# Optimization experiments

Hardware: AMD Instinct MI355X
Metric: run time of the kernel (lower is better)

## Reference

```python
import jax, jax.numpy as jnp
import numpy as np

N = 50000   # nodes
E = 800000  # edges
D = 128     # input_dim == hidden_dim
R = 8       # num_relations
B = 2       # num_blocks


def setup_inputs() -> dict:
    key = jax.random.key(0)
    ks = jax.random.split(key, 9)
    x = jax.random.normal(ks[0], (N, D), dtype=jnp.float32)
    edge_index = jax.random.randint(ks[1], (2, E), 0, N, dtype=jnp.int32)
    edge_type = jax.random.randint(ks[2], (E,), 0, R, dtype=jnp.int32)
    s_blk = 1.0 / np.sqrt(D // B)
    s_root = 1.0 / np.sqrt(D)
    W1 = jax.random.normal(ks[3], (R, B, D // B, D // B), dtype=jnp.float32) * s_blk
    root1 = jax.random.normal(ks[4], (D, D), dtype=jnp.float32) * s_root
    b1 = jnp.zeros((D,), dtype=jnp.float32)
    W2 = jax.random.normal(ks[5], (R, B, D // B, D // B), dtype=jnp.float32) * s_blk
    root2 = jax.random.normal(ks[6], (D, D), dtype=jnp.float32) * s_root
    b2 = jnp.zeros((D,), dtype=jnp.float32)
    return {"x": x, "edge_index": edge_index, "edge_type": edge_type,
            "W1": W1, "root1": root1, "b1": b1,
            "W2": W2, "root2": root2, "b2": b2}


def rgcn_conv(x, src, dst, etype, W, root, bias):
    # PyG RGCNConv (num_blocks mode): per-relation MEAN aggregation of source
    # features, block-diagonal transform, summed over relations, plus root + bias.
    # Transform is linear, so aggregate first (saves per-edge matmuls).
    n = x.shape[0]
    r, b, ib, ob = W.shape
    xs = x[src]                                   # [E, d_in] gather
    seg = dst * r + etype                          # fused (node, relation) id
    sums = jax.ops.segment_sum(xs, seg, num_segments=n * r)        # [n*r, d_in]
    cnt = jax.ops.segment_sum(jnp.ones((xs.shape[0],), xs.dtype), seg,
                              num_segments=n * r)                   # [n*r]
    mean = sums / jnp.maximum(cnt, 1.0)[:, None]   # zero where no edges
    agg = mean.reshape(n, r, b, ib)                # [n, R, blocks, in/blocks]
    out = jnp.einsum('nrbc,rbcd->nbd', agg, W).reshape(n, b * ob)
    return out + x @ root + bias


def reference(x, edge_index, edge_type, W1, root1, b1, W2, root2, b2):
    src, dst = edge_index[0], edge_index[1]
    h = jax.nn.relu(rgcn_conv(x, src, dst, edge_type, W1, root1, b1))
    # dropout(p=0.2) is identity in eval mode (reference uses eval semantics)
    return rgcn_conv(h, src, dst, edge_type, W2, root2, b2)
```

## Files before the change

kernel.cpp:

```cpp
#include <hip/hip_runtime.h>

#define NN 50000
#define EE 800000
#define DD 128
#define RR 8
#define CELLS (NN * RR)
#define TILE_N 64
#define NBLK ((NN + TILE_N - 1) / TILE_N)
#define SCAN_CHUNK 1024
#define SCAN_BLOCKS ((CELLS + SCAN_CHUNK - 1) / SCAN_CHUNK)

typedef __attribute__((ext_vector_type(4))) float f32x4;
typedef __attribute__((ext_vector_type(8))) short s16x8;
union ABu { uint4 q; s16x8 v; };


__device__ __forceinline__ unsigned int packbf2(float a, float b) {
    unsigned int ua = __float_as_uint(a);
    unsigned int ub = __float_as_uint(b);
    ua = (ua + 0x7fffu + ((ua >> 16) & 1u)) >> 16;
    ub = (ub + 0x7fffu + ((ub >> 16) & 1u)) & 0xffff0000u;
    return ua | ub;
}

__device__ __forceinline__ void upadd16(float* sA, uint4 a, uint4 b) {
    unsigned int u[8] = {a.x, a.y, a.z, a.w, b.x, b.y, b.z, b.w};
#pragma unroll
    for (int j = 0; j < 8; ++j) {
        sA[2 * j]     += __uint_as_float(u[j] << 16);
        sA[2 * j + 1] += __uint_as_float(u[j] & 0xffff0000u);
    }
}

#define NB_A ((NN * 32 + 255) / 256)
#define NB_B 128
#define NB_C 32
#define NB_D ((EE + 255) / 256)

__global__ void prep_fused(const float* __restrict__ x, unsigned int* __restrict__ xb,
                           const float* __restrict__ W1, const float* __restrict__ W2,
                           unsigned int* __restrict__ Wb1, unsigned int* __restrict__ Wb2,
                           const float* __restrict__ r1, const float* __restrict__ r2,
                           unsigned int* __restrict__ rb1, unsigned int* __restrict__ rb2,
                           const int* __restrict__ dst, const int* __restrict__ et,
                           int* __restrict__ cnt) {
    int bid = blockIdx.x, tid = threadIdx.x;
    if (bid < NB_A) {
        int i = bid * 256 + tid;
        if (i < NN * 32) {
            float4 v = ((const float4*)x)[i];
            ((uint2*)xb)[i] = make_uint2(packbf2(v.x, v.y), packbf2(v.z, v.w));
        }
    } else if (bid < NB_A + NB_B) {
        int i = (bid - NB_A) * 256 + tid;
        int kp = i & 31, n = (i >> 5) & 63, rb = i >> 11;
        int s0 = (rb * 64 + 2 * kp) * 64 + n;
        int s1 = (rb * 64 + 2 * kp + 1) * 64 + n;
        Wb1[((rb * 64 + n) * 32) + kp] = packbf2(W1[s0], W1[s1]);
        Wb2[((rb * 64 + n) * 32) + kp] = packbf2(W2[s0], W2[s1]);
    } else if (bid < NB_A + NB_B + NB_C) {
        int i = (bid - NB_A - NB_B) * 256 + tid;
        int kp = i & 63, n = i >> 6;
        int s0 = (2 * kp) * 128 + n, s1 = (2 * kp + 1) * 128 + n;
        rb1[n * 64 + kp] = packbf2(r1[s0], r1[s1]);
        rb2[n * 64 + kp] = packbf2(r2[s0], r2[s1]);
    } else {
        int e = (bid - NB_A - NB_B - NB_C) * 256 + tid;
        if (e < EE) atomicAdd(&cnt[et[e] * NN + dst[e]], 1);
    }
}


__global__ __launch_bounds__(256) void scan1(const int* __restrict__ cnt,
                                             int* __restrict__ off, int* __restrict__ bsum) {
    __shared__ int s[256];
    int tid = threadIdx.x;
    int base = blockIdx.x * SCAN_CHUNK + tid * 4;
    int v[4];
#pragma unroll
    for (int i = 0; i < 4; ++i) v[i] = (base + i < CELLS) ? cnt[base + i] : 0;
    int tot = v[0] + v[1] + v[2] + v[3];
    s[tid] = tot;
    __syncthreads();
    for (int d = 1; d < 256; d <<= 1) {
        int t = (tid >= d) ? s[tid - d] : 0;
        __syncthreads();
        s[tid] += t;
        __syncthreads();
    }
    int excl = s[tid] - tot;
    if (tid == 255) bsum[blockIdx.x] = s[255];
    int run = excl;
#pragma unroll
    for (int i = 0; i < 4; ++i) {
        if (base + i < CELLS) off[base + i] = run;
        run += v[i];
    }
}

__global__ __launch_bounds__(256) void scan3(int* __restrict__ off, const int* __restrict__ bsum,
                                             int* __restrict__ cur) {
    __shared__ int red[256];
    int tid = threadIdx.x, bid = blockIdx.x;
    int a = 0;
    for (int i = tid; i < bid; i += 256) a += bsum[i];
    red[tid] = a;
    __syncthreads();
#pragma unroll
    for (int d = 128; d > 0; d >>= 1) {
        if (tid < d) red[tid] += red[tid + d];
        __syncthreads();
    }
    int add = red[0];
    int base = bid * SCAN_CHUNK + tid * 4;
#pragma unroll
    for (int i = 0; i < 4; ++i) {
        int c = base + i;
        if (c < CELLS) {
            int o = off[c] + add;
            off[c] = o;
            cur[c] = o;
        }
    }
    if (bid == 0 && tid == 0) off[CELLS] = EE;
}

__global__ void cell_scatter(const int* __restrict__ src, const int* __restrict__ dst,
                             const int* __restrict__ et, int* __restrict__ cur,
                             int* __restrict__ esrc) {
    int e = blockIdx.x * blockDim.x + threadIdx.x;
    if (e < EE) {
        int cell = et[e] * NN + dst[e];
        int pos = atomicAdd(&cur[cell], 1);
        esrc[pos] = src[e];
    }
}

template <int RELU, int WRITEF, int WRITEB>
__global__ __launch_bounds__(512, 4) void layer_fused(
    const unsigned int* __restrict__ xgb, const int* __restrict__ esrc,
    const int* __restrict__ off,
    const unsigned int* __restrict__ Wb, const unsigned int* __restrict__ rootb,
    const float* __restrict__ bias, float* __restrict__ outf,
    unsigned int* __restrict__ outb) {

    __shared__ unsigned int SH[8320];
    unsigned int* MT = SH;

    int tid = threadIdx.x;
    int n0 = blockIdx.x * TILE_N;
    int e = tid & 63, q = tid >> 6;
    int w = tid >> 6, l = tid & 63;
    int quad = l >> 4, li = l & 15;
    int b = w >> 2;

    f32x4 acc[4];
    {
        float bb = bias[16 * w + li];
#pragma unroll
        for (int mt = 0; mt < 4; ++mt) {
            acc[mt][0] = bb; acc[mt][1] = bb; acc[mt][2] = bb; acc[mt][3] = bb;
        }
    }

    int node = n0 + e;

    for (int r = 0; r < RR; ++r) {
        float sA[16];
#pragma unroll
        for (int i = 0; i < 16; ++i) sA[i] = 0.f;
        int ne = 0;
        if (node < NN) {
            int cell = r * NN + node;
            int o = off[cell];
            ne = off[cell + 1] - o;
            int t2 = 0;
            for (; t2 + 2 <= ne; t2 += 2) {
                int s0 = esrc[o + t2], s1 = esrc[o + t2 + 1];
                const uint4* p0 = (const uint4*)(xgb + (size_t)s0 * 64 + q * 8);
                const uint4* p1 = (const uint4*)(xgb + (size_t)s1 * 64 + q * 8);
                uint4 A0 = p0[0], A1 = p0[1];
                uint4 B0 = p1[0], B1 = p1[1];
                upadd16(sA, A0, A1);
                upadd16(sA, B0, B1);
            }
            if (t2 < ne) {
                int s0 = esrc[o + t2];
                const uint4* p0 = (const uint4*)(xgb + (size_t)s0 * 64 + q * 8);
                uint4 A0 = p0[0], A1 = p0[1];
                upadd16(sA, A0, A1);
            }
        }
        float sc = 1.0f / (float)max(ne, 1);

        __syncthreads();
#pragma unroll
        for (int i = 0; i < 8; ++i)
            MT[(8 * q + i) * 67 + e] = packbf2(sA[2 * i] * sc, sA[2 * i + 1] * sc);
        __syncthreads();

        const uint4* WbB = (const uint4*)(Wb + (((size_t)r * 2 + b) * 64) * 32);
        int nloc = (w & 3) * 16 + li;
#pragma unroll
        for (int kc = 0; kc < 2; ++kc) {
            ABu bf;
            bf.q = WbB[nloc * 8 + 4 * kc + quad];
#pragma unroll
            for (int mt = 0; mt < 4; ++mt) {
                ABu af;
                int base = (32 * b + 16 * kc + 4 * quad) * 67 + 16 * mt + li;
                af.q.x = MT[base]; af.q.y = MT[base + 67];
                af.q.z = MT[base + 134]; af.q.w = MT[base + 201];
                acc[mt] = __builtin_amdgcn_mfma_f32_16x16x32_bf16(af.v, bf.v, acc[mt], 0, 0, 0);
            }
        }
    }
    __syncthreads();

    if (node < NN) {
        const uint4* xr = (const uint4*)(xgb + (size_t)node * 64 + q * 8);
        uint4 X0 = xr[0], X1 = xr[1];
        MT[(8 * q + 0) * 67 + e] = X0.x;
        MT[(8 * q + 1) * 67 + e] = X0.y;
        MT[(8 * q + 2) * 67 + e] = X0.z;
        MT[(8 * q + 3) * 67 + e] = X0.w;
        MT[(8 * q + 4) * 67 + e] = X1.x;
        MT[(8 * q + 5) * 67 + e] = X1.y;
        MT[(8 * q + 6) * 67 + e] = X1.z;
        MT[(8 * q + 7) * 67 + e] = X1.w;
    } else {
#pragma unroll
        for (int i = 0; i < 8; ++i) MT[(8 * q + i) * 67 + e] = 0u;
    }
    __syncthreads();

    const uint4* RbB = (const uint4*)rootb;
#pragma unroll
    for (int kc = 0; kc < 4; ++kc) {
        ABu bf;
        bf.q = RbB[(16 * w + li) * 16 + 4 * kc + quad];
#pragma unroll
        for (int mt = 0; mt < 4; ++mt) {
            ABu af;
            int base = (16 * kc + 4 * quad) * 67 + 16 * mt + li;
            af.q.x = MT[base]; af.q.y = MT[base + 67];
            af.q.z = MT[base + 134]; af.q.w = MT[base + 201];
            acc[mt] = __builtin_amdgcn_mfma_f32_16x16x32_bf16(af.v, bf.v, acc[mt], 0, 0, 0);
        }
    }
    __syncthreads();

    float* OF = (float*)SH;
#pragma unroll
    for (int mt = 0; mt < 4; ++mt)
#pragma unroll
        for (int reg = 0; reg < 4; ++reg)
            OF[(16 * mt + 4 * quad + reg) * 130 + 16 * w + li] = acc[mt][reg];
    __syncthreads();

    if (WRITEB) {
        int p = tid & 63, rg = tid >> 6;
#pragma unroll 4
        for (int it = 0; it < 8; ++it) {
            int ee = it * 8 + rg, row = n0 + ee;
            if (row < NN) {
                float v0 = OF[ee * 130 + 2 * p], v1 = OF[ee * 130 + 2 * p + 1];
                if (RELU) { v0 = fmaxf(v0, 0.f); v1 = fmaxf(v1, 0.f); }
                outb[(size_t)row * 64 + p] = packbf2(v0, v1);
            }
        }
    }
    if (WRITEF) {
        int d4 = (tid & 31) * 4, rg = tid >> 5;
#pragma unroll 4
        for (int it = 0; it < 4; ++it) {
            int ee = it * 16 + rg, row = n0 + ee;
            if (row < NN) {
                float4 v = make_float4(OF[ee * 130 + d4], OF[ee * 130 + d4 + 1],
                                       OF[ee * 130 + d4 + 2], OF[ee * 130 + d4 + 3]);
                if (RELU) {
                    v.x = fmaxf(v.x, 0.f); v.y = fmaxf(v.y, 0.f);
                    v.z = fmaxf(v.z, 0.f); v.w = fmaxf(v.w, 0.f);
                }
                *(float4*)(outf + (size_t)row * DD + d4) = v;
            }
        }
    }
}


extern "C" void kernel_launch(void* const* d_in, const int* in_sizes, int n_in,
                              void* d_out, int out_size, void* d_ws, size_t ws_size,
                              hipStream_t stream) {
    const float* x     = (const float*)d_in[0];
    const int*   ei    = (const int*)d_in[1];
    const int*   src   = ei;
    const int*   dstp  = ei + EE;
    const int*   et    = (const int*)d_in[2];
    const float* W1    = (const float*)d_in[3];
    const float* root1 = (const float*)d_in[4];
    const float* b1    = (const float*)d_in[5];
    const float* W2    = (const float*)d_in[6];
    const float* root2 = (const float*)d_in[7];
    const float* b2    = (const float*)d_in[8];
    float* out = (float*)d_out;

    unsigned int* xb  = (unsigned int*)d_ws;
    unsigned int* hb  = xb + (size_t)NN * 64;
    int* cnt  = (int*)(hb + (size_t)NN * 64);
    int* off  = cnt + CELLS;
    int* cur  = off + CELLS + 1;
    int* bsum = cur + CELLS;
    int* esrc = bsum + 512;
    unsigned int* Wb1 = (unsigned int*)(esrc + EE);
    unsigned int* Wb2 = Wb1 + 32768;
    unsigned int* rb1 = Wb2 + 32768;
    unsigned int* rb2 = rb1 + 8192;

    hipMemsetAsync(cnt, 0, CELLS * sizeof(int), stream);
    prep_fused<<<NB_A + NB_B + NB_C + NB_D, 256, 0, stream>>>(
        x, xb, W1, W2, Wb1, Wb2, root1, root2, rb1, rb2, dstp, et, cnt);
    scan1<<<SCAN_BLOCKS, 256, 0, stream>>>(cnt, off, bsum);
    scan3<<<SCAN_BLOCKS, 256, 0, stream>>>(off, bsum, cur);
    cell_scatter<<<(EE + 255) / 256, 256, 0, stream>>>(src, dstp, et, cur, esrc);

    layer_fused<1, 0, 1><<<NBLK, 512, 0, stream>>>(xb, esrc, off, Wb1, rb1, b1,
                                                   nullptr, hb);
    layer_fused<0, 1, 0><<<NBLK, 512, 0, stream>>>(hb, esrc, off, Wb2, rb2, b2,
                                                   out, nullptr);
}
```

Before: 366.5 us.

## Split fused layer into separate gather kernel and GEMM kernel via workspace

```diff
diff --git a/kernel.cpp b/kernel.cpp
--- a/kernel.cpp
+++ b/kernel.cpp
@@ -53,14 +53,14 @@
         }
     } else if (bid < NB_A + NB_B) {
         int i = (bid - NB_A) * 256 + tid;
-        int kp = i & 31, n = (i >> 5) & 63, rb = i >> 11;
+        int n = i & 63, kp = (i >> 6) & 31, rb = i >> 11;
         int s0 = (rb * 64 + 2 * kp) * 64 + n;
         int s1 = (rb * 64 + 2 * kp + 1) * 64 + n;
         Wb1[((rb * 64 + n) * 32) + kp] = packbf2(W1[s0], W1[s1]);
         Wb2[((rb * 64 + n) * 32) + kp] = packbf2(W2[s0], W2[s1]);
     } else if (bid < NB_A + NB_B + NB_C) {
         int i = (bid - NB_A - NB_B) * 256 + tid;
-        int kp = i & 63, n = i >> 6;
+        int n = i & 127, kp = i >> 7;
         int s0 = (2 * kp) * 128 + n, s1 = (2 * kp + 1) * 128 + n;
         rb1[n * 64 + kp] = packbf2(r1[s0], r1[s1]);
         rb2[n * 64 + kp] = packbf2(r2[s0], r2[s1]);
@@ -136,10 +136,54 @@
     }
 }
 
+__global__ __launch_bounds__(512, 8) void gather_cells(
+    const unsigned int* __restrict__ xgb, const int* __restrict__ esrc,
+    const int* __restrict__ off, unsigned int* __restrict__ AT) {
+
+    int bid = blockIdx.x;
+    int r = bid / NBLK, tb = bid - r * NBLK;
+    int n0 = tb * TILE_N;
+    int tid = threadIdx.x;
+    int e = tid & 63, q = tid >> 6;
+    int node = n0 + e;
+
+    float sA[16];
+#pragma unroll
+    for (int i = 0; i < 16; ++i) sA[i] = 0.f;
+
+    int ne = 0;
+    if (node < NN) {
+        int cell = r * NN + node;
+        int o = off[cell];
+        ne = off[cell + 1] - o;
+        int t2 = 0;
+        for (; t2 + 2 <= ne; t2 += 2) {
+            int s0 = esrc[o + t2], s1 = esrc[o + t2 + 1];
+            const uint4* p0 = (const uint4*)(xgb + (size_t)s0 * 64 + q * 8);
+            const uint4* p1 = (const uint4*)(xgb + (size_t)s1 * 64 + q * 8);
+            uint4 A0 = p0[0], A1 = p0[1];
+            uint4 B0 = p1[0], B1 = p1[1];
+            upadd16(sA, A0, A1);
+            upadd16(sA, B0, B1);
+        }
+        if (t2 < ne) {
+            int s0 = esrc[o + t2];
+            const uint4* p0 = (const uint4*)(xgb + (size_t)s0 * 64 + q * 8);
+            uint4 A0 = p0[0], A1 = p0[1];
+            upadd16(sA, A0, A1);
+        }
+    }
+    float sc = 1.0f / (float)max(ne, 1);
+
+    unsigned int* dst = AT + ((size_t)bid << 12);
+#pragma unroll
+    for (int i = 0; i < 8; ++i)
+        dst[(8 * q + i) * 64 + e] = packbf2(sA[2 * i] * sc, sA[2 * i + 1] * sc);
+}
+
 template <int RELU, int WRITEF, int WRITEB>
-__global__ __launch_bounds__(512, 4) void layer_fused(
-    const unsigned int* __restrict__ xgb, const int* __restrict__ esrc,
-    const int* __restrict__ off,
+__global__ __launch_bounds__(512, 4) void gemm_fused(
+    const unsigned int* __restrict__ xgb, const unsigned int* __restrict__ AT,
     const unsigned int* __restrict__ Wb, const unsigned int* __restrict__ rootb,
     const float* __restrict__ bias, float* __restrict__ outf,
     unsigned int* __restrict__ outb) {
@@ -148,11 +192,13 @@
     unsigned int* MT = SH;
 
     int tid = threadIdx.x;
-    int n0 = blockIdx.x * TILE_N;
+    int tb = blockIdx.x;
+    int n0 = tb * TILE_N;
     int e = tid & 63, q = tid >> 6;
-    int w = tid >> 6, l = tid & 63;
+    int w = q, l = e;
     int quad = l >> 4, li = l & 15;
     int b = w >> 2;
+    int nloc = (w & 3) * 16 + li;
 
     f32x4 acc[4];
     {
@@ -165,55 +211,29 @@
 
     int node = n0 + e;
 
+#define MFMA_BLOCK(rr) do {                                                           \
+    const uint4* WbB = (const uint4*)(Wb + (((size_t)(rr) * 2 + b) * 64) * 32);       \
+    _Pragma("unroll") for (int kc = 0; kc < 2; ++kc) {                                \
+        ABu bf; bf.q = WbB[nloc * 8 + 4 * kc + quad];                                 \
+        _Pragma("unroll") for (int mt = 0; mt < 4; ++mt) {                            \
+            ABu af; int base_ = (32 * b + 16 * kc + 4 * quad) * 67 + 16 * mt + li;    \
+            af.q.x = MT[base_];       af.q.y = MT[base_ + 67];                        \
+            af.q.z = MT[base_ + 134]; af.q.w = MT[base_ + 201];                       \
+            acc[mt] = __builtin_amdgcn_mfma_f32_16x16x32_bf16(af.v, bf.v, acc[mt], 0, 0, 0); \
+        } } } while (0)
+
+#pragma unroll
     for (int r = 0; r < RR; ++r) {
-        float sA[16];
-#pragma unroll
-        for (int i = 0; i < 16; ++i) sA[i] = 0.f;
-        int ne = 0;
-        if (node < NN) {
-            int cell = r * NN + node;
-            int o = off[cell];
-            ne = off[cell + 1] - o;
-            int t2 = 0;
-            for (; t2 + 2 <= ne; t2 += 2) {
-                int s0 = esrc[o + t2], s1 = esrc[o + t2 + 1];
-                const uint4* p0 = (const uint4*)(xgb + (size_t)s0 * 64 + q * 8);
-                const uint4* p1 = (const uint4*)(xgb + (size_t)s1 * 64 + q * 8);
-                uint4 A0 = p0[0], A1 = p0[1];
-                uint4 B0 = p1[0], B1 = p1[1];
-                upadd16(sA, A0, A1);
-                upadd16(sA, B0, B1);
-            }
-            if (t2 < ne) {
-                int s0 = esrc[o + t2];
-                const uint4* p0 = (const uint4*)(xgb + (size_t)s0 * 64 + q * 8);
-                uint4 A0 = p0[0], A1 = p0[1];
-                upadd16(sA, A0, A1);
-            }
-        }
-        float sc = 1.0f / (float)max(ne, 1);
-
-        __syncthreads();
-#pragma unroll
-        for (int i = 0; i < 8; ++i)
-            MT[(8 * q + i) * 67 + e] = packbf2(sA[2 * i] * sc, sA[2 * i + 1] * sc);
-        __syncthreads();
-
-        const uint4* WbB = (const uint4*)(Wb + (((size_t)r * 2 + b) * 64) * 32);
-        int nloc = (w & 3) * 16 + li;
-#pragma unroll
-        for (int kc = 0; kc < 2; ++kc) {
-            ABu bf;
-            bf.q = WbB[nloc * 8 + 4 * kc + quad];
-#pragma unroll
-            for (int mt = 0; mt < 4; ++mt) {
-                ABu af;
-                int base = (32 * b + 16 * kc + 4 * quad) * 67 + 16 * mt + li;
-                af.q.x = MT[base]; af.q.y = MT[base + 67];
-                af.q.z = MT[base + 134]; af.q.w = MT[base + 201];
-                acc[mt] = __builtin_amdgcn_mfma_f32_16x16x32_bf16(af.v, bf.v, acc[mt], 0, 0, 0);
-            }
-        }
+        const unsigned int* at = AT + (((size_t)(r * NBLK + tb)) << 12) + (8 * q) * 64 + e;
+        unsigned int tv[8];
+#pragma unroll
+        for (int i = 0; i < 8; ++i) tv[i] = at[i * 64];
+
+        __syncthreads();
+#pragma unroll
+        for (int i = 0; i < 8; ++i) MT[(8 * q + i) * 67 + e] = tv[i];
+        __syncthreads();
+        MFMA_BLOCK(r);
     }
     __syncthreads();
 
@@ -286,6 +306,7 @@
             }
         }
     }
+#undef MFMA_BLOCK
 }
 
 
@@ -316,6 +337,7 @@
     unsigned int* Wb2 = Wb1 + 32768;
     unsigned int* rb1 = Wb2 + 32768;
     unsigned int* rb2 = rb1 + 8192;
+    unsigned int* AT  = rb2 + 8192;
 
     hipMemsetAsync(cnt, 0, CELLS * sizeof(int), stream);
     prep_fused<<<NB_A + NB_B + NB_C + NB_D, 256, 0, stream>>>(
@@ -324,8 +346,8 @@
     scan3<<<SCAN_BLOCKS, 256, 0, stream>>>(off, bsum, cur);
     cell_scatter<<<(EE + 255) / 256, 256, 0, stream>>>(src, dstp, et, cur, esrc);
 
-    layer_fused<1, 0, 1><<<NBLK, 512, 0, stream>>>(xb, esrc, off, Wb1, rb1, b1,
-                                                   nullptr, hb);
-    layer_fused<0, 1, 0><<<NBLK, 512, 0, stream>>>(hb, esrc, off, Wb2, rb2, b2,
-                                                   out, nullptr);
-}
+    gather_cells<<<RR * NBLK, 512, 0, stream>>>(xb, esrc, off, AT);
+    gemm_fused<1, 0, 1><<<NBLK, 512, 0, stream>>>(xb, AT, Wb1, rb1, b1, nullptr, hb);
+    gather_cells<<<RR * NBLK, 512, 0, stream>>>(hb, esrc, off, AT);
+    gemm_fused<0, 1, 0><<<NBLK, 512, 0, stream>>>(hb, AT, Wb2, rb2, b2, out, nullptr);
+}
```

New measurement: 345.2 us. 5.8% less time.
